# Performance work log

Measured on AMD Instinct MI355X. Metric: run time of the kernel, lower is better.

Reference implementation:

```python
import jax, jax.numpy as jnp
from jax import lax
import numpy as np

B, L, N_NODES, EMB, TDIM, H, NCLS = 512, 200, 100000, 128, 10, 256, 2
IN = TDIM + EMB  # 138


def setup_inputs() -> dict:
    key = jax.random.key(0)
    ks = jax.random.split(key, 16)
    x = jax.random.randint(ks[0], (B, L, 2), 0, N_NODES, dtype=jnp.int64)
    s = 0.05
    inp = {
        'x': x,
        'emb_table': jax.random.normal(ks[1], (N_NODES, EMB), jnp.float32) * s,
        'ts_W': jnp.ones((1, TDIM), jnp.float32),
        'w_ih_f': jax.random.normal(ks[2], (4 * H, IN), jnp.float32) * s,
        'w_hh_f': jax.random.normal(ks[3], (4 * H, H), jnp.float32) * s,
        'b_ih_f': jax.random.normal(ks[4], (4 * H,), jnp.float32) * s,
        'b_hh_f': jax.random.normal(ks[5], (4 * H,), jnp.float32) * s,
        'w_ih_b': jax.random.normal(ks[6], (4 * H, IN), jnp.float32) * s,
        'w_hh_b': jax.random.normal(ks[7], (4 * H, H), jnp.float32) * s,
        'b_ih_b': jax.random.normal(ks[8], (4 * H,), jnp.float32) * s,
        'b_hh_b': jax.random.normal(ks[9], (4 * H,), jnp.float32) * s,
        'fc_W': jax.random.normal(ks[10], (NCLS, 2 * H), jnp.float32) * s,
        'fc_b': jax.random.normal(ks[11], (NCLS,), jnp.float32) * s,
    }
    return inp


def _lstm_dir(x_seq, w_ih, w_hh, b_ih, b_hh, reverse):
    # x_seq: [B, L, F]; PyTorch gate order i, f, g, o
    bsz = x_seq.shape[0]
    h_dim = w_hh.shape[1]
    xg = jnp.einsum('blf,gf->blg', x_seq, w_ih) + b_ih + b_hh  # [B, L, 4H]
    xs = jnp.swapaxes(xg, 0, 1)  # [L, B, 4H]
    if reverse:
        xs = xs[::-1]

    def step(carry, xg_t):
        h, c = carry
        g = xg_t + h @ w_hh.T
        i, f, gg, o = jnp.split(g, 4, axis=-1)
        c = jax.nn.sigmoid(f) * c + jax.nn.sigmoid(i) * jnp.tanh(gg)
        h = jax.nn.sigmoid(o) * jnp.tanh(c)
        return (h, c), h

    z = jnp.zeros((bsz, h_dim), x_seq.dtype)
    _, hs = lax.scan(step, (z, z), xs)
    hs = jnp.swapaxes(hs, 0, 1)  # [B, L, H]
    if reverse:
        hs = hs[:, ::-1]
    return hs


def reference(x, emb_table, ts_W, w_ih_f, w_hh_f, b_ih_f, b_hh_f,
              w_ih_b, w_hh_b, b_ih_b, b_hh_b, fc_W, fc_b):
    # timestamp embedding: [B, L, 1] @ [1, 10] -> [B, L, 10]
    t = x[:, :, 0:1].astype(jnp.float32)
    t_emb = t @ ts_W
    # F.normalize(p=2, dim=1): L2-normalize over the sequence axis
    norm = jnp.sqrt(jnp.sum(t_emb * t_emb, axis=1, keepdims=True))
    t_emb = t_emb / jnp.maximum(norm, 1e-12)

    # vectorized node-embedding gather; id == -1 -> zero vector
    ids = x[:, :, 1]
    gathered = emb_table[jnp.clip(ids, 0, None)]  # [B, L, 128]
    l_emb = jnp.where((ids >= 0)[..., None], gathered, jnp.zeros((), gathered.dtype))

    embedding = jnp.concatenate([t_emb, l_emb], axis=2)  # [B, L, 138]

    h_f = _lstm_dir(embedding, w_ih_f, w_hh_f, b_ih_f, b_hh_f, reverse=False)
    h_b = _lstm_dir(embedding, w_ih_b, w_hh_b, b_ih_b, b_hh_b, reverse=True)
    out = jnp.concatenate([h_f, h_b], axis=-1)  # [B, L, 2H]

    return out[:, -1, :] @ fc_W.T + fc_b  # [B, num_classes]
```

## Files before the change

kernel.cpp:

```cpp
#include <hip/hip_runtime.h>
#include <stdint.h>


typedef unsigned short u16;
typedef __bf16 bf16x8 __attribute__((ext_vector_type(8)));
typedef float  f32x4  __attribute__((ext_vector_type(4)));
typedef int    i32x4v __attribute__((ext_vector_type(4)));
typedef int    i32x8v __attribute__((ext_vector_type(8)));

#define B_    512
#define L_    200
#define EMB_  128
#define TDIM_ 10
#define IN_   138
#define INP_  160
#define H_    256
#define G4_   1024
#define T_    200
#define DS_   (1.0f/1024.0f)
#define LOG2E 1.4426950408889634f
#define EXP2(x) __builtin_amdgcn_exp2f(x)

static __device__ __forceinline__ float bf2f(u16 u) {
  union { uint32_t i; float f; } v; v.i = ((uint32_t)u) << 16; return v.f;
}
static __device__ __forceinline__ u16 f2bf(float f) {
  __bf16 h = (__bf16)f; return __builtin_bit_cast(u16, h);
}
static __device__ __forceinline__ float bflo(uint32_t u) {
  return __builtin_bit_cast(float, (uint32_t)(u << 16));
}
static __device__ __forceinline__ float bfhi(uint32_t u) {
  return __builtin_bit_cast(float, (uint32_t)(u & 0xffff0000u));
}
static __device__ __forceinline__ float sigf(float x) {
  return __builtin_amdgcn_rcpf(1.0f + EXP2(-x * LOG2E));
}
static __device__ __forceinline__ float tanh_(float x) {
  x = fminf(fmaxf(x, -15.f), 15.f);
  float e = EXP2(2.0f * LOG2E * x);
  return (e - 1.0f) * __builtin_amdgcn_rcpf(e + 1.0f);
}
static __device__ __forceinline__ f32x4 mfma16(bf16x8 a, bf16x8 b, f32x4 c) {
  return __builtin_amdgcn_mfma_f32_16x16x32_bf16(a, b, c, 0, 0, 0);
}
static __device__ __forceinline__ f32x4 vzero4() {
  f32x4 v; v[0] = 0.f; v[1] = 0.f; v[2] = 0.f; v[3] = 0.f; return v;
}

__global__ void k_norm(const int* __restrict__ x, float* __restrict__ s) {
  int b = blockIdx.x;
  int tid = threadIdx.x;
  float v = 0.f;
  if (tid < L_) {
    float t = (float)x[(b * L_ + tid) * 2];
    v = t * t;
  }
  #pragma unroll
  for (int o = 32; o; o >>= 1) v += __shfl_down(v, o);
  __shared__ float p[4];
  if ((tid & 63) == 0) p[tid >> 6] = v;
  __syncthreads();
  if (tid == 0) s[b] = p[0] + p[1] + p[2] + p[3];
}

__global__ void k_prep_mx(const float* __restrict__ whh, int* __restrict__ wf8) {
  int idx = blockIdx.x * blockDim.x + threadIdx.x;
  int d = idx & 7;
  int lane = (idx >> 3) & 63;
  int fs = idx >> 9;
  int kp2 = fs & 1, tt = (fs >> 1) & 7, w = fs >> 4;
  int mm = lane & 15, q = lane >> 4;
  int g = (w + 8 * tt) * 16 + mm;
  int k = kp2 * 128 + q * 32 + d * 4;
  const float* src = whh + g * 256 + k;
  int v = __builtin_amdgcn_cvt_pk_fp8_f32(src[0] * 64.f, src[1] * 64.f, 0, false);
  v     = __builtin_amdgcn_cvt_pk_fp8_f32(src[2] * 64.f, src[3] * 64.f, v, true);
  wf8[idx] = v;
}

__global__ void k_feat(const int* __restrict__ x, const float* __restrict__ emb,
                       const float* __restrict__ tsW, const float* __restrict__ s,
                       u16* __restrict__ feat) {
  int idx = blockIdx.x * blockDim.x + threadIdx.x;
  if (idx >= B_ * L_ * INP_) return;
  int c = idx % INP_;
  int row = idx / INP_;
  int b = row / L_;
  float v = 0.f;
  if (c < TDIM_) {
    float t = (float)x[row * 2 + 0];
    float wd = tsW[c];
    float den = fmaxf(fabsf(wd) * sqrtf(s[b]), 1e-12f);
    v = t * wd / den;
  } else if (c < IN_) {
    int id = x[row * 2 + 1];
    int idc = id < 0 ? 0 : id;
    float e = emb[(long)idc * EMB_ + (c - TDIM_)];
    v = (id >= 0) ? e : 0.f;
  }
  feat[idx] = f2bf(v);
}

__global__ __launch_bounds__(512, 2) void k_xg(
    const u16* __restrict__ feat, const float* __restrict__ wih,
    const float* __restrict__ bih, const float* __restrict__ bhh,
    u16* __restrict__ xg) {
  __shared__ u16 Bs[256 * 176];
  const int nt = blockIdx.x;
  const int mt = blockIdx.y;
  const int tid = threadIdx.x;
  const int w = tid >> 6, lane = tid & 63;
  const int q = lane >> 4, nm = lane & 15;
  for (int i2 = tid; i2 < 256 * 88; i2 += 512) {
    int gl = i2 / 88, f2 = (i2 % 88) * 2;
    int pk = 0;
    if (f2 < IN_) {
      float2 v = *(const float2*)(wih + (long)(nt * 256 + gl) * IN_ + f2);
      pk = (int)f2bf(v.x) | ((int)f2bf(v.y) << 16);
    }
    *(int*)&Bs[gl * 176 + f2] = pk;
  }
  float bias[16];
  #pragma unroll
  for (int nu = 0; nu < 16; ++nu) {
    int g = nt * 256 + nu * 16 + nm;
    bias[nu] = bih[g] + bhh[g];
  }
  __syncthreads();
  f32x4 acc[2][16];
  #pragma unroll
  for (int m = 0; m < 2; ++m)
    #pragma unroll
    for (int nu = 0; nu < 16; ++nu) acc[m][nu] = vzero4();
  const u16* arow = feat + (long)(mt * 256 + w * 32) * INP_;
  #pragma unroll
  for (int kp = 0; kp < 5; ++kp) {
    bf16x8 a0 = *(const bf16x8*)(arow + (nm * INP_ + kp * 32 + q * 8));
    bf16x8 a1 = *(const bf16x8*)(arow + ((16 + nm) * INP_ + kp * 32 + q * 8));
    #pragma unroll
    for (int nu = 0; nu < 16; ++nu) {
      bf16x8 bb = *(const bf16x8*)&Bs[(nu * 16 + nm) * 176 + kp * 32 + q * 8];
      acc[0][nu] = mfma16(a0, bb, acc[0][nu]);
      acc[1][nu] = mfma16(a1, bb, acc[1][nu]);
    }
  }
  u16* Os = Bs;
  #pragma unroll
  for (int p = 0; p < 2; ++p) {
    __syncthreads();
    if ((w >> 2) == p) {
      #pragma unroll
      for (int nu = 0; nu < 16; ++nu)
        #pragma unroll
        for (int m = 0; m < 2; ++m)
          #pragma unroll
          for (int r = 0; r < 4; ++r) {
            int row = (w & 3) * 32 + m * 16 + 4 * q + r;
            Os[row * 264 + nu * 16 + nm] = f2bf((acc[m][nu][r] + bias[nu]) * 1024.f);
          }
    }
    __syncthreads();
    #pragma unroll
    for (int it = 0; it < 8; ++it) {
      int flat = it * 512 + tid;
      int row = flat >> 5, c = flat & 31;
      uint4 v = *(const uint4*)&Os[row * 264 + c * 8];
      *(uint4*)&xg[(long)(mt * 256 + p * 128 + row) * G4_ + nt * 256 + c * 8] = v;
    }
  }
}

#define MX2A(accv, A0, A1, Bx, By) \
  asm volatile("v_mfma_f32_16x16x128_f8f6f4 %0, %1, %3, %0\n\t" \
               "v_mfma_f32_16x16x128_f8f6f4 %0, %2, %4, %0" \
               : "+v"(accv) : "a"(A0), "a"(A1), "v"(Bx), "v"(By));
#define AINIT(i) \
  f32x4 acc##i; acc##i[0] = bflo(pf##i.x); acc##i[1] = bfhi(pf##i.x); \
  acc##i[2] = bflo(pf##i.y); acc##i[3] = bfhi(pf##i.y);
#define PFL(i) pf##i = *(const uint2*)(xn + ((w + 8 * (i)) * 16 + 4 * q));
#define EPIROW(r, cs, aI, aF, aG, aO, hv) { \
  float ei = EXP2((aI)[r] * c_sig); \
  float ef = EXP2((aF)[r] * c_sig); \
  float eo = EXP2((aO)[r] * c_sig); \
  float eg = EXP2(fminf((aG)[r] * c_tg, 126.f)); \
  float c  = cs[r] * __builtin_amdgcn_rcpf(1.f + ef) \
           + (eg - 1.f) * __builtin_amdgcn_rcpf((1.f + ei) * (1.f + eg)); \
  cs[r] = c; \
  float ec = EXP2(fminf(c * c_tc, 126.f)); \
  (hv)[r] = (ec - 1.f) * __builtin_amdgcn_rcpf((1.f + eo) * (1.f + ec)); }
#define HPACK(jj, hv) { \
  int pk = __builtin_amdgcn_cvt_pk_fp8_f32((hv)[0] * 16.f, (hv)[1] * 16.f, 0, false); \
  pk     = __builtin_amdgcn_cvt_pk_fp8_f32((hv)[2] * 16.f, (hv)[3] * 16.f, pk, true); \
  hw[nn * 68 + 4 * w + 32 * (jj) + q] = pk; \
  if (t == T_ - 1) *(f32x4*)&hf[(long)b * H_ + 16 * w + 128 * (jj) + 4 * q] = (hv); }

__global__ __launch_bounds__(512, 2) void k_lstm_f(
    const int* __restrict__ wf8, const u16* __restrict__ xg,
    float* __restrict__ hf) {
  __shared__ int hls[2][16 * 68];
  const int tid = threadIdx.x;
  const int w = tid >> 6;
  const int lane = tid & 63;
  const int q = lane >> 4;
  const int nn = lane & 15;
  const int b = blockIdx.x * 16 + nn;
  const float c_sig = -DS_ * LOG2E;
  const float c_tg  = 2.f * DS_ * LOG2E;
  const float c_tc  = 2.f * LOG2E;

#define WREG(fi) (*(const i32x8v*)(wf8 + (long)((w * 16 + (fi)) * 64 + lane) * 8))
  i32x8v W00 = WREG(0),  W01 = WREG(1),  W10 = WREG(2),  W11 = WREG(3);
  i32x8v W20 = WREG(4),  W21 = WREG(5),  W30 = WREG(6),  W31 = WREG(7);
  i32x8v W40 = WREG(8),  W41 = WREG(9),  W50 = WREG(10), W51 = WREG(11);
  i32x8v W60 = WREG(12), W61 = WREG(13), W70 = WREG(14), W71 = WREG(15);
  for (int i = tid; i < 16 * 68; i += 512) hls[0][i] = 0;

  const u16* xgb = xg + (long)b * (L_ * G4_);
  uint2 pf0, pf1, pf2, pf3, pf4, pf5, pf6, pf7;
  {
    const u16* xn = xgb;
    PFL(0) PFL(1) PFL(2) PFL(3) PFL(4) PFL(5) PFL(6) PFL(7)
  }
  f32x4 cst0 = vzero4(), cst1 = vzero4();
  __syncthreads();

  #pragma unroll 1
  for (int t = 0; t < T_; ++t) {
    AINIT(0) AINIT(1) AINIT(2) AINIT(3) AINIT(4) AINIT(5) AINIT(6) AINIT(7)
    {
      const u16* xn = xgb + (long)(t + 1 < T_ ? t + 1 : t) * G4_;
      PFL(0) PFL(1) PFL(2) PFL(3) PFL(4) PFL(5) PFL(6) PFL(7)
    }
    const int* hr = hls[t & 1];
    i32x8v B0 = __builtin_shufflevector(
        *(const i32x4v*)&hr[nn * 68 + q * 8],
        *(const i32x4v*)&hr[nn * 68 + q * 8 + 4], 0, 1, 2, 3, 4, 5, 6, 7);
    i32x8v B1 = __builtin_shufflevector(
        *(const i32x4v*)&hr[nn * 68 + 32 + q * 8],
        *(const i32x4v*)&hr[nn * 68 + 32 + q * 8 + 4], 0, 1, 2, 3, 4, 5, 6, 7);
    MX2A(acc0, W00, W01, B0, B1);
    MX2A(acc2, W20, W21, B0, B1);
    MX2A(acc4, W40, W41, B0, B1);
    MX2A(acc6, W60, W61, B0, B1);
    MX2A(acc1, W10, W11, B0, B1);
    MX2A(acc3, W30, W31, B0, B1);
    asm volatile("s_nop 7\n\ts_nop 7"
                 : "+v"(acc0), "+v"(acc2), "+v"(acc4), "+v"(acc6));
    int* hw = hls[1 - (t & 1)];
    f32x4 hv0;
    EPIROW(0, cst0, acc0, acc2, acc4, acc6, hv0)
    MX2A(acc5, W50, W51, B0, B1);
    EPIROW(1, cst0, acc0, acc2, acc4, acc6, hv0)
    MX2A(acc7, W70, W71, B0, B1);
    EPIROW(2, cst0, acc0, acc2, acc4, acc6, hv0)
    EPIROW(3, cst0, acc0, acc2, acc4, acc6, hv0)
    HPACK(0, hv0)
    asm volatile("s_nop 7\n\ts_nop 7"
                 : "+v"(acc1), "+v"(acc3), "+v"(acc5), "+v"(acc7));
    f32x4 hv1;
    EPIROW(0, cst1, acc1, acc3, acc5, acc7, hv1)
    EPIROW(1, cst1, acc1, acc3, acc5, acc7, hv1)
    EPIROW(2, cst1, acc1, acc3, acc5, acc7, hv1)
    EPIROW(3, cst1, acc1, acc3, acc5, acc7, hv1)
    HPACK(1, hv1)
    __asm__ volatile("" ::: "memory");
    __builtin_amdgcn_s_waitcnt(0xc07f);
    __builtin_amdgcn_s_barrier();
    __asm__ volatile("" ::: "memory");
  }
}

__global__ __launch_bounds__(256) void k_bwd(
    const u16* __restrict__ feat, const float* __restrict__ wih,
    const float* __restrict__ bih, const float* __restrict__ bhh,
    float* __restrict__ hb) {
  const int b0 = blockIdx.x * 8;
  const int tid = threadIdx.x;
  __shared__ float fv[8][IN_];
  for (int i = tid; i < 8 * IN_; i += 256) {
    int r = i / IN_, c = i % IN_;
    fv[r][c] = bf2f(feat[((long)(b0 + r) * L_ + (L_ - 1)) * INP_ + c]);
  }
  __syncthreads();
  float gi[8], gg[8], go[8];
  float bi_ = bih[tid] + bhh[tid];
  float bg_ = bih[2 * H_ + tid] + bhh[2 * H_ + tid];
  float bo_ = bih[3 * H_ + tid] + bhh[3 * H_ + tid];
  #pragma unroll
  for (int r = 0; r < 8; ++r) { gi[r] = bi_; gg[r] = bg_; go[r] = bo_; }
  const float* wi_ = wih + (long)tid * IN_;
  const float* wg_ = wih + (long)(2 * H_ + tid) * IN_;
  const float* wo_ = wih + (long)(3 * H_ + tid) * IN_;
  for (int f = 0; f < IN_; ++f) {
    float a = wi_[f], gc = wg_[f], oc = wo_[f];
    #pragma unroll
    for (int r = 0; r < 8; ++r) {
      float x = fv[r][f];
      gi[r] += a * x;
      gg[r] += gc * x;
      go[r] += oc * x;
    }
  }
  #pragma unroll
  for (int r = 0; r < 8; ++r) {
    float c = sigf(gi[r]) * tanh_(gg[r]);
    hb[(long)(b0 + r) * H_ + tid] = sigf(go[r]) * tanh_(c);
  }
}

__global__ void k_fc(const float* __restrict__ hf, const float* __restrict__ hb,
                     const float* __restrict__ fcw, const float* __restrict__ fcb,
                     float* __restrict__ out) {
  int b = blockIdx.x;
  int lane = threadIdx.x;
  float p0 = 0.f, p1 = 0.f;
  #pragma unroll
  for (int k = lane; k < 2 * H_; k += 64) {
    float v = (k < H_) ? hf[b * H_ + k] : hb[b * H_ + (k - H_)];
    p0 += v * fcw[k];
    p1 += v * fcw[2 * H_ + k];
  }
  #pragma unroll
  for (int o = 32; o; o >>= 1) {
    p0 += __shfl_down(p0, o);
    p1 += __shfl_down(p1, o);
  }
  if (lane == 0) {
    out[b * 2 + 0] = p0 + fcb[0];
    out[b * 2 + 1] = p1 + fcb[1];
  }
}

extern "C" void kernel_launch(void* const* d_in, const int* in_sizes, int n_in,
                              void* d_out, int out_size, void* d_ws, size_t ws_size,
                              hipStream_t stream) {
  const int*   x    = (const int*)  d_in[0];
  const float* emb  = (const float*)d_in[1];
  const float* tsW  = (const float*)d_in[2];
  const float* wihf = (const float*)d_in[3];
  const float* whhf = (const float*)d_in[4];
  const float* bihf = (const float*)d_in[5];
  const float* bhhf = (const float*)d_in[6];
  const float* wihb = (const float*)d_in[7];
  const float* bihb = (const float*)d_in[9];
  const float* bhhb = (const float*)d_in[10];
  const float* fcw  = (const float*)d_in[11];
  const float* fcb  = (const float*)d_in[12];
  float* out = (float*)d_out;

  char* ws = (char*)d_ws;
  float* s    = (float*)(ws);
  int*   wf8  = (int*)  (ws + 2048);
  u16*   feat = (u16*)  (ws + 264192);
  u16*   xg   = (u16*)  (ws + 33032192);
  float* hf   = (float*)(ws + 242747392);
  float* hb   = (float*)(ws + 243271680);

  k_norm   <<<dim3(512),     dim3(256), 0, stream>>>(x, s);
  k_prep_mx<<<dim3(256),     dim3(256), 0, stream>>>(whhf, wf8);
  k_feat   <<<dim3(64000),   dim3(256), 0, stream>>>(x, emb, tsW, s, feat);
  k_xg     <<<dim3(4, 400),  dim3(512), 0, stream>>>(feat, wihf, bihf, bhhf, xg);
  k_lstm_f <<<dim3(32),      dim3(512), 0, stream>>>(wf8, xg, hf);
  k_bwd    <<<dim3(64),      dim3(256), 0, stream>>>(feat, wihb, bihb, bhhb, hb);
  k_fc     <<<dim3(512),     dim3(64),  0, stream>>>(hf, hb, fcw, fcb, out);
}
```

Before: 798.8 us.

## Widen forward LSTM to 16 waves, fuse norm into feat and bwd into lstm

The forward LSTM recurrence now runs 1024 threads per block, so each wave handles four gate tiles instead of eight. Part of the fp8 recurrent weights is kept in LDS to limit register pressure, and the epilogue is reworked to process pairs of values. The separate backward single-step kernel becomes extra blocks of the LSTM launch, so it runs alongside the recurrence, and the sequence-norm kernel is folded into a per-batch feature kernel. This aims to shorten the serial per-step critical path and cut launch count, at the cost of more block-wide barrier participants and LDS weight reads on every step.

```diff
diff --git a/kernel.cpp b/kernel.cpp
--- a/kernel.cpp
+++ b/kernel.cpp
@@ -5,6 +5,7 @@
 typedef unsigned short u16;
 typedef __bf16 bf16x8 __attribute__((ext_vector_type(8)));
 typedef float  f32x4  __attribute__((ext_vector_type(4)));
+typedef float  f32x2  __attribute__((ext_vector_type(2)));
 typedef int    i32x4v __attribute__((ext_vector_type(4)));
 typedef int    i32x8v __attribute__((ext_vector_type(8)));
 
@@ -20,6 +21,7 @@
 #define DS_   (1.0f/1024.0f)
 #define LOG2E 1.4426950408889634f
 #define EXP2(x) __builtin_amdgcn_exp2f(x)
+#define RCP(x)  __builtin_amdgcn_rcpf(x)
 
 static __device__ __forceinline__ float bf2f(u16 u) {
   union { uint32_t i; float f; } v; v.i = ((uint32_t)u) << 16; return v.f;
@@ -34,34 +36,18 @@
   return __builtin_bit_cast(float, (uint32_t)(u & 0xffff0000u));
 }
 static __device__ __forceinline__ float sigf(float x) {
-  return __builtin_amdgcn_rcpf(1.0f + EXP2(-x * LOG2E));
+  return RCP(1.0f + EXP2(-x * LOG2E));
 }
 static __device__ __forceinline__ float tanh_(float x) {
   x = fminf(fmaxf(x, -15.f), 15.f);
   float e = EXP2(2.0f * LOG2E * x);
-  return (e - 1.0f) * __builtin_amdgcn_rcpf(e + 1.0f);
+  return (e - 1.0f) * RCP(e + 1.0f);
 }
 static __device__ __forceinline__ f32x4 mfma16(bf16x8 a, bf16x8 b, f32x4 c) {
   return __builtin_amdgcn_mfma_f32_16x16x32_bf16(a, b, c, 0, 0, 0);
 }
 static __device__ __forceinline__ f32x4 vzero4() {
   f32x4 v; v[0] = 0.f; v[1] = 0.f; v[2] = 0.f; v[3] = 0.f; return v;
-}
-
-__global__ void k_norm(const int* __restrict__ x, float* __restrict__ s) {
-  int b = blockIdx.x;
-  int tid = threadIdx.x;
-  float v = 0.f;
-  if (tid < L_) {
-    float t = (float)x[(b * L_ + tid) * 2];
-    v = t * t;
-  }
-  #pragma unroll
-  for (int o = 32; o; o >>= 1) v += __shfl_down(v, o);
-  __shared__ float p[4];
-  if ((tid & 63) == 0) p[tid >> 6] = v;
-  __syncthreads();
-  if (tid == 0) s[b] = p[0] + p[1] + p[2] + p[3];
 }
 
 __global__ void k_prep_mx(const float* __restrict__ whh, int* __restrict__ wf8) {
@@ -79,27 +65,40 @@
   wf8[idx] = v;
 }
 
-__global__ void k_feat(const int* __restrict__ x, const float* __restrict__ emb,
-                       const float* __restrict__ tsW, const float* __restrict__ s,
-                       u16* __restrict__ feat) {
-  int idx = blockIdx.x * blockDim.x + threadIdx.x;
-  if (idx >= B_ * L_ * INP_) return;
-  int c = idx % INP_;
-  int row = idx / INP_;
-  int b = row / L_;
+__global__ __launch_bounds__(256) void k_feat(
+    const int* __restrict__ x, const float* __restrict__ emb,
+    const float* __restrict__ tsW, u16* __restrict__ feat) {
+  __shared__ float sh_t[224];
+  __shared__ int   sh_id[224];
+  __shared__ float sh_s[4];
+  const int b = blockIdx.x, tid = threadIdx.x;
   float v = 0.f;
-  if (c < TDIM_) {
-    float t = (float)x[row * 2 + 0];
-    float wd = tsW[c];
-    float den = fmaxf(fabsf(wd) * sqrtf(s[b]), 1e-12f);
-    v = t * wd / den;
-  } else if (c < IN_) {
-    int id = x[row * 2 + 1];
-    int idc = id < 0 ? 0 : id;
-    float e = emb[(long)idc * EMB_ + (c - TDIM_)];
-    v = (id >= 0) ? e : 0.f;
-  }
-  feat[idx] = f2bf(v);
+  if (tid < L_) {
+    int2 p = *(const int2*)&x[(b * L_ + tid) * 2];
+    float t = (float)p.x;
+    sh_t[tid] = t;
+    sh_id[tid] = p.y;
+    v = t * t;
+  }
+  #pragma unroll
+  for (int o = 32; o; o >>= 1) v += __shfl_down(v, o);
+  if ((tid & 63) == 0) sh_s[tid >> 6] = v;
+  __syncthreads();
+  const float sq = sqrtf(sh_s[0] + sh_s[1] + sh_s[2] + sh_s[3]);
+  for (int i = tid; i < L_ * INP_; i += 256) {
+    int l = i / INP_, c = i - l * INP_;
+    float v2 = 0.f;
+    if (c < TDIM_) {
+      float wd = tsW[c];
+      float den = fmaxf(fabsf(wd) * sq, 1e-12f);
+      v2 = sh_t[l] * wd * RCP(den);
+    } else if (c < IN_) {
+      int id = sh_id[l];
+      float e = emb[(long)(id < 0 ? 0 : id) * EMB_ + (c - TDIM_)];
+      v2 = (id >= 0) ? e : 0.f;
+    }
+    feat[(long)b * (L_ * INP_) + i] = f2bf(v2);
+  }
 }
 
 __global__ __launch_bounds__(512, 2) void k_xg(
@@ -171,34 +170,84 @@
   }
 }
 
-#define MX2A(accv, A0, A1, Bx, By) \
-  asm volatile("v_mfma_f32_16x16x128_f8f6f4 %0, %1, %3, %0\n\t" \
-               "v_mfma_f32_16x16x128_f8f6f4 %0, %2, %4, %0" \
-               : "+v"(accv) : "a"(A0), "a"(A1), "v"(Bx), "v"(By));
+#define F8MA(accv, Aa, Bv) \
+  asm volatile("v_mfma_f32_16x16x128_f8f6f4 %0, %1, %2, %0" \
+               : "+v"(accv) : "a"(Aa), "v"(Bv));
+#define F8MV(accv, Av, Bv) \
+  asm volatile("v_mfma_f32_16x16x128_f8f6f4 %0, %1, %2, %0" \
+               : "+v"(accv) : "v"(Av), "v"(Bv));
 #define AINIT(i) \
   f32x4 acc##i; acc##i[0] = bflo(pf##i.x); acc##i[1] = bfhi(pf##i.x); \
   acc##i[2] = bflo(pf##i.y); acc##i[3] = bfhi(pf##i.y);
-#define PFL(i) pf##i = *(const uint2*)(xn + ((w + 8 * (i)) * 16 + 4 * q));
-#define EPIROW(r, cs, aI, aF, aG, aO, hv) { \
-  float ei = EXP2((aI)[r] * c_sig); \
-  float ef = EXP2((aF)[r] * c_sig); \
-  float eo = EXP2((aO)[r] * c_sig); \
-  float eg = EXP2(fminf((aG)[r] * c_tg, 126.f)); \
-  float c  = cs[r] * __builtin_amdgcn_rcpf(1.f + ef) \
-           + (eg - 1.f) * __builtin_amdgcn_rcpf((1.f + ei) * (1.f + eg)); \
-  cs[r] = c; \
-  float ec = EXP2(fminf(c * c_tc, 126.f)); \
-  (hv)[r] = (ec - 1.f) * __builtin_amdgcn_rcpf((1.f + eo) * (1.f + ec)); }
-#define HPACK(jj, hv) { \
-  int pk = __builtin_amdgcn_cvt_pk_fp8_f32((hv)[0] * 16.f, (hv)[1] * 16.f, 0, false); \
-  pk     = __builtin_amdgcn_cvt_pk_fp8_f32((hv)[2] * 16.f, (hv)[3] * 16.f, pk, true); \
-  hw[nn * 68 + 4 * w + 32 * (jj) + q] = pk; \
-  if (t == T_ - 1) *(f32x4*)&hf[(long)b * H_ + 16 * w + 128 * (jj) + 4 * q] = (hv); }
-
-__global__ __launch_bounds__(512, 2) void k_lstm_f(
+#define PFL(i, ptr) pf##i = *(const uint2*)((ptr) + (16 * (w + 16 * (i)) + 4 * q));
+#define EPIPAIR(P, cs2, hv2) f32x2 hv2; { \
+  f32x2 ai = {acc0[2*(P)], acc0[2*(P)+1]}; \
+  f32x2 af = {acc1[2*(P)], acc1[2*(P)+1]}; \
+  f32x2 ag = {acc2[2*(P)], acc2[2*(P)+1]}; \
+  f32x2 ao = {acc3[2*(P)], acc3[2*(P)+1]}; \
+  f32x2 xi = ai * c_sig, xf = af * c_sig, xo = ao * c_sig, xgv = ag * c_tg; \
+  f32x2 ei, ef, eo, eg, ec; \
+  ei[0] = EXP2(xi[0]); ei[1] = EXP2(xi[1]); \
+  ef[0] = EXP2(xf[0]); ef[1] = EXP2(xf[1]); \
+  eo[0] = EXP2(xo[0]); eo[1] = EXP2(xo[1]); \
+  eg[0] = EXP2(xgv[0]); eg[1] = EXP2(xgv[1]); \
+  f32x2 t1 = ef + 1.f; \
+  f32x2 r1; r1[0] = RCP(t1[0]); r1[1] = RCP(t1[1]); \
+  f32x2 t2 = (ei + 1.f) * (eg + 1.f); \
+  f32x2 r2; r2[0] = RCP(t2[0]); r2[1] = RCP(t2[1]); \
+  f32x2 c = cs2 * r1 + (eg - 1.f) * r2; \
+  cs2 = c; \
+  f32x2 xc = c * c_tc; \
+  ec[0] = EXP2(xc[0]); ec[1] = EXP2(xc[1]); \
+  f32x2 t3 = (eo + 1.f) * (ec + 1.f); \
+  f32x2 r3; r3[0] = RCP(t3[0]); r3[1] = RCP(t3[1]); \
+  hv2 = (ec * 16.f - 16.f) * r3; }
+
+#define FSOLD(M, kp2) (((M) & 7) * 16 + ((M) >> 3) * 2 + (kp2))
+#define WLOAD(M, kp2) (*(const i32x8v*)(wf8 + ((long)(FSOLD(M, kp2)) * 64 + lane) * 8))
+
+__global__ __launch_bounds__(1024, 4) void k_lstm_f(
     const int* __restrict__ wf8, const u16* __restrict__ xg,
-    float* __restrict__ hf) {
+    float* __restrict__ hf,
+    const u16* __restrict__ feat, const float* __restrict__ wihb,
+    const float* __restrict__ bihb, const float* __restrict__ bhhb,
+    float* __restrict__ hb) {
+  __shared__ i32x8v ldsW[32 * 64];
   __shared__ int hls[2][16 * 68];
+
+  if (blockIdx.x >= 32) {
+    const int b0 = (blockIdx.x - 32) * 8;
+    const int tid = threadIdx.x;
+    float* fv = (float*)hls;
+    for (int i = tid; i < 8 * IN_; i += 1024) {
+      int r = i / IN_, c = i - r * IN_;
+      fv[r * IN_ + c] = bf2f(feat[((long)(b0 + r) * L_ + (L_ - 1)) * INP_ + c]);
+    }
+    __syncthreads();
+    const int col = tid & 255, rq = tid >> 8;
+    float gi0 = bihb[col] + bhhb[col];
+    float gg0 = bihb[512 + col] + bhhb[512 + col];
+    float go0 = bihb[768 + col] + bhhb[768 + col];
+    float gi1 = gi0, gg1 = gg0, go1 = go0;
+    const float* wi_ = wihb + (long)col * IN_;
+    const float* wg_ = wihb + (long)(512 + col) * IN_;
+    const float* wo_ = wihb + (long)(768 + col) * IN_;
+    const float* f0 = fv + (rq * 2) * IN_;
+    const float* f1 = fv + (rq * 2 + 1) * IN_;
+    for (int f = 0; f < IN_; ++f) {
+      float a = wi_[f], g = wg_[f], o = wo_[f];
+      float x0 = f0[f], x1 = f1[f];
+      gi0 += a * x0; gi1 += a * x1;
+      gg0 += g * x0; gg1 += g * x1;
+      go0 += o * x0; go1 += o * x1;
+    }
+    float c0 = sigf(gi0) * tanh_(gg0);
+    float c1 = sigf(gi1) * tanh_(gg1);
+    hb[(long)(b0 + rq * 2) * H_ + col]     = sigf(go0) * tanh_(c0);
+    hb[(long)(b0 + rq * 2 + 1) * H_ + col] = sigf(go1) * tanh_(c1);
+    return;
+  }
+
   const int tid = threadIdx.x;
   const int w = tid >> 6;
   const int lane = tid & 63;
@@ -209,103 +258,52 @@
   const float c_tg  = 2.f * DS_ * LOG2E;
   const float c_tc  = 2.f * LOG2E;
 
-#define WREG(fi) (*(const i32x8v*)(wf8 + (long)((w * 16 + (fi)) * 64 + lane) * 8))
-  i32x8v W00 = WREG(0),  W01 = WREG(1),  W10 = WREG(2),  W11 = WREG(3);
-  i32x8v W20 = WREG(4),  W21 = WREG(5),  W30 = WREG(6),  W31 = WREG(7);
-  i32x8v W40 = WREG(8),  W41 = WREG(9),  W50 = WREG(10), W51 = WREG(11);
-  i32x8v W60 = WREG(12), W61 = WREG(13), W70 = WREG(14), W71 = WREG(15);
-  for (int i = tid; i < 16 * 68; i += 512) hls[0][i] = 0;
+  i32x8v A00 = WLOAD(w, 0),      A01 = WLOAD(w, 1);
+  i32x8v A10 = WLOAD(w + 16, 0), A11 = WLOAD(w + 16, 1);
+  i32x8v A20 = WLOAD(w + 32, 0), A21 = WLOAD(w + 32, 1);
+  ldsW[(w * 2 + 0) * 64 + lane] = WLOAD(w + 48, 0);
+  ldsW[(w * 2 + 1) * 64 + lane] = WLOAD(w + 48, 1);
+  for (int i = tid; i < 16 * 68; i += 1024) hls[0][i] = 0;
 
   const u16* xgb = xg + (long)b * (L_ * G4_);
-  uint2 pf0, pf1, pf2, pf3, pf4, pf5, pf6, pf7;
-  {
-    const u16* xn = xgb;
-    PFL(0) PFL(1) PFL(2) PFL(3) PFL(4) PFL(5) PFL(6) PFL(7)
-  }
-  f32x4 cst0 = vzero4(), cst1 = vzero4();
+  uint2 pf0, pf1, pf2, pf3;
+  PFL(0, xgb) PFL(1, xgb) PFL(2, xgb) PFL(3, xgb)
+  f32x2 cs0; cs0[0] = 0.f; cs0[1] = 0.f;
+  f32x2 cs1; cs1[0] = 0.f; cs1[1] = 0.f;
   __syncthreads();
 
   #pragma unroll 1
   for (int t = 0; t < T_; ++t) {
-    AINIT(0) AINIT(1) AINIT(2) AINIT(3) AINIT(4) AINIT(5) AINIT(6) AINIT(7)
+    const int* hr = hls[t & 1];
+    i32x8v B0 = *(const i32x8v*)&hr[nn * 68 + q * 8];
+    i32x8v B1 = *(const i32x8v*)&hr[nn * 68 + 32 + q * 8];
+    i32x8v L0 = ldsW[(w * 2 + 0) * 64 + lane];
+    i32x8v L1 = ldsW[(w * 2 + 1) * 64 + lane];
+    AINIT(0) AINIT(1) AINIT(2) AINIT(3)
     {
       const u16* xn = xgb + (long)(t + 1 < T_ ? t + 1 : t) * G4_;
-      PFL(0) PFL(1) PFL(2) PFL(3) PFL(4) PFL(5) PFL(6) PFL(7)
-    }
-    const int* hr = hls[t & 1];
-    i32x8v B0 = __builtin_shufflevector(
-        *(const i32x4v*)&hr[nn * 68 + q * 8],
-        *(const i32x4v*)&hr[nn * 68 + q * 8 + 4], 0, 1, 2, 3, 4, 5, 6, 7);
-    i32x8v B1 = __builtin_shufflevector(
-        *(const i32x4v*)&hr[nn * 68 + 32 + q * 8],
-        *(const i32x4v*)&hr[nn * 68 + 32 + q * 8 + 4], 0, 1, 2, 3, 4, 5, 6, 7);
-    MX2A(acc0, W00, W01, B0, B1);
-    MX2A(acc2, W20, W21, B0, B1);
-    MX2A(acc4, W40, W41, B0, B1);
-    MX2A(acc6, W60, W61, B0, B1);
-    MX2A(acc1, W10, W11, B0, B1);
-    MX2A(acc3, W30, W31, B0, B1);
+      PFL(0, xn) PFL(1, xn) PFL(2, xn) PFL(3, xn)
+    }
+    F8MA(acc0, A00, B0) F8MA(acc1, A10, B0) F8MA(acc2, A20, B0) F8MV(acc3, L0, B0)
+    F8MA(acc0, A01, B1) F8MA(acc1, A11, B1) F8MA(acc2, A21, B1) F8MV(acc3, L1, B1)
     asm volatile("s_nop 7\n\ts_nop 7"
-                 : "+v"(acc0), "+v"(acc2), "+v"(acc4), "+v"(acc6));
+                 : "+v"(acc0), "+v"(acc1), "+v"(acc2), "+v"(acc3));
     int* hw = hls[1 - (t & 1)];
-    f32x4 hv0;
-    EPIROW(0, cst0, acc0, acc2, acc4, acc6, hv0)
-    MX2A(acc5, W50, W51, B0, B1);
-    EPIROW(1, cst0, acc0, acc2, acc4, acc6, hv0)
-    MX2A(acc7, W70, W71, B0, B1);
-    EPIROW(2, cst0, acc0, acc2, acc4, acc6, hv0)
-    EPIROW(3, cst0, acc0, acc2, acc4, acc6, hv0)
-    HPACK(0, hv0)
-    asm volatile("s_nop 7\n\ts_nop 7"
-                 : "+v"(acc1), "+v"(acc3), "+v"(acc5), "+v"(acc7));
-    f32x4 hv1;
-    EPIROW(0, cst1, acc1, acc3, acc5, acc7, hv1)
-    EPIROW(1, cst1, acc1, acc3, acc5, acc7, hv1)
-    EPIROW(2, cst1, acc1, acc3, acc5, acc7, hv1)
-    EPIROW(3, cst1, acc1, acc3, acc5, acc7, hv1)
-    HPACK(1, hv1)
+    EPIPAIR(0, cs0, hv0)
+    EPIPAIR(1, cs1, hv1)
+    int pk = __builtin_amdgcn_cvt_pk_fp8_f32(hv0[0], hv0[1], 0, false);
+    pk     = __builtin_amdgcn_cvt_pk_fp8_f32(hv1[0], hv1[1], pk, true);
+    hw[nn * 68 + 4 * w + q] = pk;
+    if (t == T_ - 1) {
+      f32x4 ov;
+      ov[0] = hv0[0] * 0.0625f; ov[1] = hv0[1] * 0.0625f;
+      ov[2] = hv1[0] * 0.0625f; ov[3] = hv1[1] * 0.0625f;
+      *(f32x4*)&hf[(long)b * H_ + 16 * w + 4 * q] = ov;
+    }
     __asm__ volatile("" ::: "memory");
     __builtin_amdgcn_s_waitcnt(0xc07f);
     __builtin_amdgcn_s_barrier();
     __asm__ volatile("" ::: "memory");
-  }
-}
-
-__global__ __launch_bounds__(256) void k_bwd(
-    const u16* __restrict__ feat, const float* __restrict__ wih,
-    const float* __restrict__ bih, const float* __restrict__ bhh,
-    float* __restrict__ hb) {
-  const int b0 = blockIdx.x * 8;
-  const int tid = threadIdx.x;
-  __shared__ float fv[8][IN_];
-  for (int i = tid; i < 8 * IN_; i += 256) {
-    int r = i / IN_, c = i % IN_;
-    fv[r][c] = bf2f(feat[((long)(b0 + r) * L_ + (L_ - 1)) * INP_ + c]);
-  }
-  __syncthreads();
-  float gi[8], gg[8], go[8];
-  float bi_ = bih[tid] + bhh[tid];
-  float bg_ = bih[2 * H_ + tid] + bhh[2 * H_ + tid];
-  float bo_ = bih[3 * H_ + tid] + bhh[3 * H_ + tid];
-  #pragma unroll
-  for (int r = 0; r < 8; ++r) { gi[r] = bi_; gg[r] = bg_; go[r] = bo_; }
-  const float* wi_ = wih + (long)tid * IN_;
-  const float* wg_ = wih + (long)(2 * H_ + tid) * IN_;
-  const float* wo_ = wih + (long)(3 * H_ + tid) * IN_;
-  for (int f = 0; f < IN_; ++f) {
-    float a = wi_[f], gc = wg_[f], oc = wo_[f];
-    #pragma unroll
-    for (int r = 0; r < 8; ++r) {
-      float x = fv[r][f];
-      gi[r] += a * x;
-      gg[r] += gc * x;
-      go[r] += oc * x;
-    }
-  }
-  #pragma unroll
-  for (int r = 0; r < 8; ++r) {
-    float c = sigf(gi[r]) * tanh_(gg[r]);
-    hb[(long)(b0 + r) * H_ + tid] = sigf(go[r]) * tanh_(c);
   }
 }
 
@@ -350,18 +348,16 @@
   float* out = (float*)d_out;
 
   char* ws = (char*)d_ws;
-  float* s    = (float*)(ws);
   int*   wf8  = (int*)  (ws + 2048);
   u16*   feat = (u16*)  (ws + 264192);
   u16*   xg   = (u16*)  (ws + 33032192);
   float* hf   = (float*)(ws + 242747392);
   float* hb   = (float*)(ws + 243271680);
 
-  k_norm   <<<dim3(512),     dim3(256), 0, stream>>>(x, s);
-  k_prep_mx<<<dim3(256),     dim3(256), 0, stream>>>(whhf, wf8);
-  k_feat   <<<dim3(64000),   dim3(256), 0, stream>>>(x, emb, tsW, s, feat);
-  k_xg     <<<dim3(4, 400),  dim3(512), 0, stream>>>(feat, wihf, bihf, bhhf, xg);
-  k_lstm_f <<<dim3(32),      dim3(512), 0, stream>>>(wf8, xg, hf);
-  k_bwd    <<<dim3(64),      dim3(256), 0, stream>>>(feat, wihb, bihb, bhhb, hb);
-  k_fc     <<<dim3(512),     dim3(64),  0, stream>>>(hf, hb, fcw, fcb, out);
-}
+  k_prep_mx<<<dim3(256),    dim3(256),  0, stream>>>(whhf, wf8);
+  k_feat   <<<dim3(512),    dim3(256),  0, stream>>>(x, emb, tsW, feat);
+  k_xg     <<<dim3(4, 400), dim3(512),  0, stream>>>(feat, wihf, bihf, bhhf, xg);
+  k_lstm_f <<<dim3(96),     dim3(1024), 0, stream>>>(wf8, xg, hf,
+                                                     feat, wihb, bihb, bhhb, hb);
+  k_fc     <<<dim3(512),    dim3(64),   0, stream>>>(hf, hb, fcw, fcb, out);
+}
```

Measured after the change: 729.3 us. 8.7% less time.
